# Optimization experiments

Measured on AMD Instinct MI355X. Metric: run time of the kernel, lower is better.

Reference implementation:

```python
import jax, jax.numpy as jnp
import numpy as np

B, T, DIN = 4, 1024, 512
DLIN, DK, DV, NH = 1024, 1024, 1024, 16

def setup_inputs() -> dict:
    key = jax.random.key(0)
    ks = jax.random.split(key, 5)
    s = 0.02
    return {
        "data": jax.random.normal(ks[0], (B, T, DIN), dtype=jnp.float32),
        "W_in": jax.random.normal(ks[1], (DLIN, DIN + T), dtype=jnp.float32) * s,
        "W_q": jax.random.normal(ks[2], (DK, DLIN), dtype=jnp.float32) * s,
        "W_k": jax.random.normal(ks[3], (DK, DLIN), dtype=jnp.float32) * s,
        "W_v": jax.random.normal(ks[4], (DV, DLIN), dtype=jnp.float32) * s,
    }

def reference(data, W_in, W_q, W_k, W_v):
    b, t, d_in = data.shape
    nh = NH
    dk = DK // nh
    dv = DV // nh
    scale = 1.0 / np.sqrt(dk).astype(np.float32)
    # concat identity positional one-hots: [B, T, DIN + T]
    p = jnp.broadcast_to(jnp.eye(t, dtype=data.dtype), (b, t, t))
    x = jnp.concatenate([data, p], axis=-1)
    h = jnp.einsum('btc,dc->btd', x, W_in)            # [B,T,DLIN]
    q = jnp.einsum('btd,kd->btk', h, W_q).reshape(b, t, nh, dk).transpose(0, 2, 1, 3)
    k = jnp.einsum('btd,kd->btk', h, W_k).reshape(b, t, nh, dk).transpose(0, 2, 1, 3)
    v = jnp.einsum('btd,kd->btk', h, W_v).reshape(b, t, nh, dv).transpose(0, 2, 1, 3)
    dist = jnp.einsum('bhqd,bhkd->bhqk', q, k) * scale   # [B,H,T,T]
    dist = jax.nn.softmax(dist, axis=-1)
    att = jnp.einsum('bhqk,bhkd->bhqd', dist, v)         # [B,H,T,dv]
    return att.transpose(0, 2, 1, 3).reshape(b, t, DV)
```

## Files before the change

### kernel.cpp

```cpp
#include <hip/hip_runtime.h>
#include <stdint.h>


typedef __bf16 bf16x8 __attribute__((ext_vector_type(8)));
typedef float f32x4 __attribute__((ext_vector_type(4)));
typedef float f32x16 __attribute__((ext_vector_type(16)));
typedef unsigned short u16;
typedef u16 u16x8 __attribute__((ext_vector_type(8)));

#define MFMA16(a, b, c) __builtin_amdgcn_mfma_f32_16x16x32_bf16(a, b, c, 0, 0, 0)
#define MFMA32(a, b, c) __builtin_amdgcn_mfma_f32_32x32x16_bf16(a, b, c, 0, 0, 0)

using gld_src_t = const __attribute__((address_space(1))) unsigned int*;
using gld_dst_t = __attribute__((address_space(3))) unsigned int*;

__device__ __forceinline__ u16 f2bf(float f) {
  uint32_t u = __builtin_bit_cast(uint32_t, f);
  uint32_t r = (u + 0x7fffu + ((u >> 16) & 1u)) >> 16;
  return (u16)r;
}


__global__ __launch_bounds__(256) void cvt_all(
    const float* __restrict__ data, const float* __restrict__ wq,
    const float* __restrict__ wk, const float* __restrict__ wv,
    u16* __restrict__ o_data, u16* __restrict__ o_wq,
    u16* __restrict__ o_wk, u16* __restrict__ o_wv) {
  const float* s;
  u16* o;
  int n;
  switch (blockIdx.y) {
    case 0: s = data; o = o_data; n = 4096 * 512; break;
    case 1: s = wq; o = o_wq; n = 1024 * 1024; break;
    case 2: s = wk; o = o_wk; n = 1024 * 1024; break;
    default: s = wv; o = o_wv; n = 1024 * 1024; break;
  }
  int i = (blockIdx.x * 256 + threadIdx.x) * 8;
  if (i >= n) return;
  float4 a = *(const float4*)(s + i);
  float4 b = *(const float4*)(s + i + 4);
  u16x8 v;
  v[0] = f2bf(a.x); v[1] = f2bf(a.y); v[2] = f2bf(a.z); v[3] = f2bf(a.w);
  v[4] = f2bf(b.x); v[5] = f2bf(b.y); v[6] = f2bf(b.z); v[7] = f2bf(b.w);
  *(u16x8*)(o + i) = v;
}

__global__ __launch_bounds__(256) void cvt_win(const float* __restrict__ Win,
                                               u16* __restrict__ wd) {
  int i = (blockIdx.x * 256 + threadIdx.x) * 8;
  if (i >= 1024 * 512) return;
  int row = i >> 9, col = i & 511;
  const float* s = Win + (size_t)row * 1536 + col;
  float4 a = *(const float4*)s;
  float4 b = *(const float4*)(s + 4);
  u16x8 v;
  v[0] = f2bf(a.x); v[1] = f2bf(a.y); v[2] = f2bf(a.z); v[3] = f2bf(a.w);
  v[4] = f2bf(b.x); v[5] = f2bf(b.y); v[6] = f2bf(b.z); v[7] = f2bf(b.w);
  *(u16x8*)(wd + i) = v;
}


template <int EPI>
__global__ __launch_bounds__(256) void gemm_bt(
    const u16* __restrict__ A, const u16* __restrict__ B0,
    const u16* __restrict__ B1, const u16* __restrict__ B2,
    const float* __restrict__ Wpos, u16* __restrict__ O0,
    u16* __restrict__ O1, u16* __restrict__ O2, int K) {
  __shared__ u16 Ash[128 * 64];
  __shared__ u16 Bsh[128 * 64];
  const int tid = threadIdx.x;
  const int lane = tid & 63;
  const int w = tid >> 6;
  const int wr = w >> 1, wc = w & 1;
  const int m0 = blockIdx.x * 128, n0 = blockIdx.y * 128;

  const u16* Bw;
  u16* Out;
  if constexpr (EPI == 0) {
    Bw = B0; Out = O0;
  } else {
    int z = blockIdx.z;
    Bw = (z == 0) ? B0 : (z == 1) ? B1 : B2;
    Out = (z == 0) ? O0 : (z == 1) ? O1 : O2;
  }

  f32x4 acc[4][4];
#pragma unroll
  for (int m = 0; m < 4; ++m)
#pragma unroll
    for (int n = 0; n < 4; ++n) acc[m][n] = (f32x4){0.f, 0.f, 0.f, 0.f};

  for (int kt = 0; kt < K; kt += 64) {
    __syncthreads();
#pragma unroll
    for (int i = 0; i < 4; ++i) {
      int c = i * 256 + tid;
      int row = c >> 3;
      int sg = (c & 7) ^ (row & 7);
      const u16* srcA = A + (size_t)(m0 + row) * K + kt + sg * 8;
      __builtin_amdgcn_global_load_lds((gld_src_t)srcA,
                                       (gld_dst_t)&Ash[(i * 256 + w * 64) * 8],
                                       16, 0, 0);
      const u16* srcB = Bw + (size_t)(n0 + row) * K + kt + sg * 8;
      __builtin_amdgcn_global_load_lds((gld_src_t)srcB,
                                       (gld_dst_t)&Bsh[(i * 256 + w * 64) * 8],
                                       16, 0, 0);
    }
    __syncthreads();
#pragma unroll
    for (int kk = 0; kk < 2; ++kk) {
      bf16x8 af[4], bfr[4];
#pragma unroll
      for (int m = 0; m < 4; ++m) {
        int r = wr * 64 + m * 16 + (lane & 15);
        int slot = (kk * 4 + (lane >> 4)) ^ (r & 7);
        af[m] = *(const bf16x8*)((const char*)Ash + r * 128 + slot * 16);
      }
#pragma unroll
      for (int n = 0; n < 4; ++n) {
        int r = wc * 64 + n * 16 + (lane & 15);
        int slot = (kk * 4 + (lane >> 4)) ^ (r & 7);
        bfr[n] = *(const bf16x8*)((const char*)Bsh + r * 128 + slot * 16);
      }
#pragma unroll
      for (int m = 0; m < 4; ++m)
#pragma unroll
        for (int n = 0; n < 4; ++n) acc[m][n] = MFMA16(af[m], bfr[n], acc[m][n]);
    }
  }

#pragma unroll
  for (int m = 0; m < 4; ++m) {
#pragma unroll
    for (int n = 0; n < 4; ++n) {
      int r0 = m0 + wr * 64 + m * 16 + ((lane >> 4) << 2);
      int col = n0 + wc * 64 + n * 16 + (lane & 15);
      if constexpr (EPI == 0) {
        int t0 = r0 & 1023;
        float4 pb = *(const float4*)(Wpos + (size_t)col * 1536 + 512 + t0);
        float pbv[4] = {pb.x, pb.y, pb.z, pb.w};
#pragma unroll
        for (int q = 0; q < 4; ++q)
          Out[(size_t)(r0 + q) * 1024 + col] = f2bf(acc[m][n][q] + pbv[q]);
      } else {
        float qsc = (blockIdx.z == 0) ? 0.18033688011112042f : 1.0f;
        int hd = col >> 6, j = col & 63;
        int b = r0 >> 10;
        size_t bh = (size_t)(b * 16 + hd) * 65536;
#pragma unroll
        for (int q = 0; q < 4; ++q) {
          int t = (r0 + q) & 1023;
          int tp = (t & ~12) | ((t & 4) << 1) | ((t & 8) >> 1);
          size_t idx = (blockIdx.z == 2) ? bh + (size_t)j * 1024 + tp
                                         : bh + (size_t)t * 64 + j;
          Out[idx] = f2bf(acc[m][n][q] * qsc);
        }
      }
    }
  }
}

__global__ __launch_bounds__(256, 2) void attn(const u16* __restrict__ Q,
                                               const u16* __restrict__ K,
                                               const u16* __restrict__ Vt,
                                               float* __restrict__ out) {
  __shared__ float lbuf[4][32 * 66];
  const int tid = threadIdx.x, lane = tid & 63, w = tid >> 6;
  const int q = lane & 31, hi = lane >> 5;
  const int flat = blockIdx.x;
  const int bh = (flat & 7) * 8 + ((flat >> 3) & 7);
  const int q0 = (flat >> 6) * 128 + w * 32;
  const size_t base = (size_t)bh * 65536;

  bf16x8 qf[4];
#pragma unroll
  for (int ks = 0; ks < 4; ++ks)
    qf[ks] = *(const bf16x8*)(Q + base + (size_t)(q0 + q) * 64 + ks * 16 + hi * 8);

  f32x16 ot[2];
#pragma unroll
  for (int r = 0; r < 16; ++r) {
    ot[0][r] = 0.f;
    ot[1][r] = 0.f;
  }
  float lsum = 0.f;

  const u16* Kp = K + base + (size_t)q * 64 + hi * 8;
  const u16* Vp = Vt + base + (size_t)q * 1024 + hi * 8;

  auto loadK = [&](int kv0, bf16x8 (&kb)[4]) {
#pragma unroll
    for (int ks = 0; ks < 4; ++ks)
      kb[ks] = *(const bf16x8*)(Kp + (size_t)kv0 * 64 + ks * 16);
  };
  auto loadV = [&](int kv0, bf16x8 (&vb)[4]) {
#pragma unroll
    for (int s = 0; s < 2; ++s)
#pragma unroll
      for (int d = 0; d < 2; ++d)
        vb[2 * s + d] =
            *(const bf16x8*)(Vp + (size_t)(32 * d) * 1024 + kv0 + 16 * s);
  };
  auto compute = [&](const bf16x8 (&kb)[4], const bf16x8 (&vb)[4]) {
    f32x16 st;
#pragma unroll
    for (int r = 0; r < 16; ++r) st[r] = 0.f;
#pragma unroll
    for (int ks = 0; ks < 4; ++ks) st = MFMA32(kb[ks], qf[ks], st);
    float pe[16];
#pragma unroll
    for (int r = 0; r < 16; ++r) pe[r] = __builtin_exp2f(st[r]);
    {
      float t0 = (pe[0] + pe[1]) + (pe[2] + pe[3]);
      float t1 = (pe[4] + pe[5]) + (pe[6] + pe[7]);
      float t2 = (pe[8] + pe[9]) + (pe[10] + pe[11]);
      float t3 = (pe[12] + pe[13]) + (pe[14] + pe[15]);
      lsum += (t0 + t1) + (t2 + t3);
    }
#pragma unroll
    for (int s = 0; s < 2; ++s) {
      bf16x8 pf;
#pragma unroll
      for (int j = 0; j < 8; ++j) pf[j] = (__bf16)pe[8 * s + j];
#pragma unroll
      for (int d = 0; d < 2; ++d) ot[d] = MFMA32(vb[2 * s + d], pf, ot[d]);
    }
  };

  bf16x8 kA[4], vA[4], kB[4], vB[4];
  loadK(0, kA);
  loadV(0, vA);
  for (int kv0 = 0; kv0 < 1024; kv0 += 64) {
    loadK(kv0 + 32, kB);
    loadV(kv0 + 32, vB);
    compute(kA, vA);
    if (kv0 + 64 < 1024) {
      loadK(kv0 + 64, kA);
      loadV(kv0 + 64, vA);
    }
    compute(kB, vB);
  }

  lsum += __shfl_xor(lsum, 32, 64);
  float ri = 1.0f / lsum;

  float* lb = &lbuf[w][0];
#pragma unroll
  for (int d = 0; d < 2; ++d)
#pragma unroll
    for (int rr = 0; rr < 16; rr += 2) {
      int dv = 32 * d + (rr & 3) + 8 * (rr >> 2) + 4 * hi;
      *(float2*)(lb + q * 66 + dv) =
          make_float2(ot[d][rr] * ri, ot[d][rr + 1] * ri);
    }
  __syncthreads();
  const int b = bh >> 4, hd = bh & 15;
#pragma unroll
  for (int i = 0; i < 8; ++i) {
    int row = i * 4 + (lane >> 4);
    const float* lr = lb + row * 66 + (lane & 15) * 4;
    float2 x0 = *(const float2*)lr;
    float2 x1 = *(const float2*)(lr + 2);
    float4 v = make_float4(x0.x, x0.y, x1.x, x1.y);
    *(float4*)(out + ((size_t)(b * 1024 + q0 + row)) * 1024 + hd * 64 +
               (lane & 15) * 4) = v;
  }
}


extern "C" void kernel_launch(void* const* d_in, const int* in_sizes, int n_in,
                              void* d_out, int out_size, void* d_ws,
                              size_t ws_size, hipStream_t stream) {
  const float* data = (const float*)d_in[0];
  const float* Win = (const float*)d_in[1];
  const float* Wq = (const float*)d_in[2];
  const float* Wk = (const float*)d_in[3];
  const float* Wv = (const float*)d_in[4];
  float* out = (float*)d_out;

  char* ws = (char*)d_ws;
  u16* data_b = (u16*)ws; ws += (size_t)4096 * 512 * 2;
  u16* wd_b = (u16*)ws;   ws += (size_t)1024 * 512 * 2;
  u16* wq_b = (u16*)ws;   ws += (size_t)1024 * 1024 * 2;
  u16* wk_b = (u16*)ws;   ws += (size_t)1024 * 1024 * 2;
  u16* wv_b = (u16*)ws;   ws += (size_t)1024 * 1024 * 2;
  u16* h_b = (u16*)ws;    ws += (size_t)4096 * 1024 * 2;
  u16* q_b = (u16*)ws;    ws += (size_t)4194304 * 2;
  u16* k_b = (u16*)ws;    ws += (size_t)4194304 * 2;
  u16* vt_b = (u16*)ws;   ws += (size_t)4194304 * 2;

  cvt_all<<<dim3(1024, 4), 256, 0, stream>>>(data, Wq, Wk, Wv, data_b, wq_b,
                                             wk_b, wv_b);
  cvt_win<<<dim3(256), 256, 0, stream>>>(Win, wd_b);
  gemm_bt<0><<<dim3(32, 8, 1), 256, 0, stream>>>(data_b, wd_b, wd_b, wd_b, Win,
                                                 h_b, h_b, h_b, 512);
  gemm_bt<1><<<dim3(32, 8, 3), 256, 0, stream>>>(h_b, wq_b, wk_b, wv_b, nullptr,
                                                 q_b, k_b, vt_b, 1024);
  attn<<<dim3(512), 256, 0, stream>>>(q_b, k_b, vt_b, out);
}
```

Baseline: 193.6 us.

## Switch attention to 16x16 MFMA tiles with smaller per-wave query blocks

Rewrites the attention kernel to use 16x16x32 MFMA instead of 32x32x16, so each wave handles 16 queries instead of 32, and doubles the grid to 1024 blocks. The V-transpose permutation in the QKV GEMM epilogue is changed to match the new fragment layout. Launch bounds rise to 4 blocks per CU, and the epilogue uses float4 LDS stores and loads. The aim is smaller register footprint, higher occupancy and more blocks for latency hiding. The cost is that each K/V element is loaded twice as often across waves, since each wave covers fewer queries.

```diff
diff --git a/kernel.cpp b/kernel.cpp
--- a/kernel.cpp
+++ b/kernel.cpp
@@ -4,12 +4,10 @@
 
 typedef __bf16 bf16x8 __attribute__((ext_vector_type(8)));
 typedef float f32x4 __attribute__((ext_vector_type(4)));
-typedef float f32x16 __attribute__((ext_vector_type(16)));
 typedef unsigned short u16;
 typedef u16 u16x8 __attribute__((ext_vector_type(8)));
 
 #define MFMA16(a, b, c) __builtin_amdgcn_mfma_f32_16x16x32_bf16(a, b, c, 0, 0, 0)
-#define MFMA32(a, b, c) __builtin_amdgcn_mfma_f32_32x32x16_bf16(a, b, c, 0, 0, 0)
 
 using gld_src_t = const __attribute__((address_space(1))) unsigned int*;
 using gld_dst_t = __attribute__((address_space(3))) unsigned int*;
@@ -150,7 +148,9 @@
 #pragma unroll
         for (int q = 0; q < 4; ++q) {
           int t = (r0 + q) & 1023;
-          int tp = (t & ~12) | ((t & 4) << 1) | ((t & 8) >> 1);
+          int kv5 = t & 31;
+          int tp = (t & ~31) | (((kv5 >> 2) & 3) * 8 + ((kv5 >> 4) & 1) * 4 +
+                                (kv5 & 3));
           size_t idx = (blockIdx.z == 2) ? bh + (size_t)j * 1024 + tp
                                          : bh + (size_t)t * 64 + j;
           Out[idx] = f2bf(acc[m][n][q] * qsc);
@@ -160,29 +160,27 @@
   }
 }
 
-__global__ __launch_bounds__(256, 2) void attn(const u16* __restrict__ Q,
+__global__ __launch_bounds__(256, 4) void attn(const u16* __restrict__ Q,
                                                const u16* __restrict__ K,
                                                const u16* __restrict__ Vt,
                                                float* __restrict__ out) {
-  __shared__ float lbuf[4][32 * 66];
+  __shared__ float lbuf[4][16 * 68];
   const int tid = threadIdx.x, lane = tid & 63, w = tid >> 6;
-  const int q = lane & 31, hi = lane >> 5;
+  const int q = lane & 15, hi = lane >> 4;
   const int flat = blockIdx.x;
   const int bh = (flat & 7) * 8 + ((flat >> 3) & 7);
-  const int q0 = (flat >> 6) * 128 + w * 32;
+  const int q0w = (flat >> 6) * 64 + w * 16;
   const size_t base = (size_t)bh * 65536;
 
-  bf16x8 qf[4];
-#pragma unroll
-  for (int ks = 0; ks < 4; ++ks)
-    qf[ks] = *(const bf16x8*)(Q + base + (size_t)(q0 + q) * 64 + ks * 16 + hi * 8);
-
-  f32x16 ot[2];
-#pragma unroll
-  for (int r = 0; r < 16; ++r) {
-    ot[0][r] = 0.f;
-    ot[1][r] = 0.f;
-  }
+  bf16x8 qf[2];
+#pragma unroll
+  for (int ks = 0; ks < 2; ++ks)
+    qf[ks] =
+        *(const bf16x8*)(Q + base + (size_t)(q0w + q) * 64 + ks * 32 + hi * 8);
+
+  f32x4 od[4];
+#pragma unroll
+  for (int d = 0; d < 4; ++d) od[d] = (f32x4){0.f, 0.f, 0.f, 0.f};
   float lsum = 0.f;
 
   const u16* Kp = K + base + (size_t)q * 64 + hi * 8;
@@ -190,80 +188,79 @@
 
   auto loadK = [&](int kv0, bf16x8 (&kb)[4]) {
 #pragma unroll
-    for (int ks = 0; ks < 4; ++ks)
-      kb[ks] = *(const bf16x8*)(Kp + (size_t)kv0 * 64 + ks * 16);
+    for (int u = 0; u < 2; ++u)
+#pragma unroll
+      for (int ks = 0; ks < 2; ++ks)
+        kb[u * 2 + ks] =
+            *(const bf16x8*)(Kp + (size_t)(kv0 + u * 16) * 64 + ks * 32);
   };
   auto loadV = [&](int kv0, bf16x8 (&vb)[4]) {
 #pragma unroll
-    for (int s = 0; s < 2; ++s)
-#pragma unroll
-      for (int d = 0; d < 2; ++d)
-        vb[2 * s + d] =
-            *(const bf16x8*)(Vp + (size_t)(32 * d) * 1024 + kv0 + 16 * s);
+    for (int d = 0; d < 4; ++d)
+      vb[d] = *(const bf16x8*)(Vp + (size_t)(d * 16) * 1024 + kv0);
   };
   auto compute = [&](const bf16x8 (&kb)[4], const bf16x8 (&vb)[4]) {
-    f32x16 st;
-#pragma unroll
-    for (int r = 0; r < 16; ++r) st[r] = 0.f;
-#pragma unroll
-    for (int ks = 0; ks < 4; ++ks) st = MFMA32(kb[ks], qf[ks], st);
-    float pe[16];
-#pragma unroll
-    for (int r = 0; r < 16; ++r) pe[r] = __builtin_exp2f(st[r]);
-    {
-      float t0 = (pe[0] + pe[1]) + (pe[2] + pe[3]);
-      float t1 = (pe[4] + pe[5]) + (pe[6] + pe[7]);
-      float t2 = (pe[8] + pe[9]) + (pe[10] + pe[11]);
-      float t3 = (pe[12] + pe[13]) + (pe[14] + pe[15]);
-      lsum += (t0 + t1) + (t2 + t3);
-    }
-#pragma unroll
-    for (int s = 0; s < 2; ++s) {
-      bf16x8 pf;
-#pragma unroll
-      for (int j = 0; j < 8; ++j) pf[j] = (__bf16)pe[8 * s + j];
-#pragma unroll
-      for (int d = 0; d < 2; ++d) ot[d] = MFMA32(vb[2 * s + d], pf, ot[d]);
-    }
+    f32x4 s[2];
+#pragma unroll
+    for (int u = 0; u < 2; ++u) {
+      s[u] = (f32x4){0.f, 0.f, 0.f, 0.f};
+      s[u] = MFMA16(kb[u * 2 + 0], qf[0], s[u]);
+      s[u] = MFMA16(kb[u * 2 + 1], qf[1], s[u]);
+    }
+    float pe[8];
+#pragma unroll
+    for (int r = 0; r < 4; ++r) {
+      pe[r] = __builtin_exp2f(s[0][r]);
+      pe[4 + r] = __builtin_exp2f(s[1][r]);
+    }
+    lsum += ((pe[0] + pe[1]) + (pe[2] + pe[3])) +
+            ((pe[4] + pe[5]) + (pe[6] + pe[7]));
+    bf16x8 pf;
+#pragma unroll
+    for (int j = 0; j < 8; ++j) pf[j] = (__bf16)pe[j];
+#pragma unroll
+    for (int d = 0; d < 4; ++d) od[d] = MFMA16(vb[d], pf, od[d]);
   };
 
   bf16x8 kA[4], vA[4], kB[4], vB[4];
   loadK(0, kA);
   loadV(0, vA);
+  asm volatile("" ::: "memory");
   for (int kv0 = 0; kv0 < 1024; kv0 += 64) {
     loadK(kv0 + 32, kB);
     loadV(kv0 + 32, vB);
+    asm volatile("" ::: "memory");
     compute(kA, vA);
     if (kv0 + 64 < 1024) {
       loadK(kv0 + 64, kA);
       loadV(kv0 + 64, vA);
+      asm volatile("" ::: "memory");
     }
     compute(kB, vB);
   }
 
+  lsum += __shfl_xor(lsum, 16, 64);
   lsum += __shfl_xor(lsum, 32, 64);
   float ri = 1.0f / lsum;
 
   float* lb = &lbuf[w][0];
 #pragma unroll
-  for (int d = 0; d < 2; ++d)
-#pragma unroll
-    for (int rr = 0; rr < 16; rr += 2) {
-      int dv = 32 * d + (rr & 3) + 8 * (rr >> 2) + 4 * hi;
-      *(float2*)(lb + q * 66 + dv) =
-          make_float2(ot[d][rr] * ri, ot[d][rr + 1] * ri);
-    }
+  for (int d = 0; d < 4; ++d) {
+    f32x4 v = od[d];
+    *(float4*)(lb + q * 68 + d * 16 + hi * 4) =
+        make_float4(v[0] * ri, v[1] * ri, v[2] * ri, v[3] * ri);
+  }
   __syncthreads();
   const int b = bh >> 4, hd = bh & 15;
-#pragma unroll
-  for (int i = 0; i < 8; ++i) {
-    int row = i * 4 + (lane >> 4);
-    const float* lr = lb + row * 66 + (lane & 15) * 4;
-    float2 x0 = *(const float2*)lr;
-    float2 x1 = *(const float2*)(lr + 2);
-    float4 v = make_float4(x0.x, x0.y, x1.x, x1.y);
-    *(float4*)(out + ((size_t)(b * 1024 + q0 + row)) * 1024 + hd * 64 +
-               (lane & 15) * 4) = v;
+  {
+    int row = lane >> 2, c0 = (lane & 3) * 16;
+    float* op = out + ((size_t)(b * 1024 + q0w + row)) * 1024 + hd * 64 + c0;
+    const float* lr = lb + row * 68 + c0;
+#pragma unroll
+    for (int i = 0; i < 4; ++i) {
+      float4 v = *(const float4*)(lr + i * 4);
+      *(float4*)(op + i * 4) = v;
+    }
   }
 }
 
@@ -296,5 +293,5 @@
                                                  h_b, h_b, h_b, 512);
   gemm_bt<1><<<dim3(32, 8, 3), 256, 0, stream>>>(h_b, wq_b, wk_b, wv_b, nullptr,
                                                  q_b, k_b, vt_b, 1024);
-  attn<<<dim3(512), 256, 0, stream>>>(q_b, k_b, vt_b, out);
-}
+  attn<<<dim3(1024), 256, 0, stream>>>(q_b, k_b, vt_b, out);
+}
```

New measurement: 246.2 us. 27.1% more time.
